# Optimization experiments

Measured on AMD Instinct MI355X. Metric: run time of the kernel, lower is better.

## Reference

```python
import jax, jax.numpy as jnp
import numpy as np

N = 200000; E = 800000; B = 4096; L = 512
DIN = 64; DE = 16; H = 128; PD = 1152


def setup_inputs() -> dict:
    key = jax.random.key(0)
    ks = jax.random.split(key, 40)
    def nrm(k, shape, fan_in):
        return jax.random.normal(k, shape, jnp.float32) * (1.0 / np.sqrt(fan_in))
    inp = {}
    inp['x'] = jax.random.normal(ks[0], (N, DIN), jnp.float32)
    inp['edge_index'] = jax.random.randint(ks[1], (2, E), 0, N, dtype=jnp.int32)
    inp['edge_attr'] = jax.random.normal(ks[2], (E, DE), jnp.float32)
    inp['batch'] = jnp.sort(jax.random.randint(ks[3], (N,), 0, B, dtype=jnp.int32))
    # 6 expert blocks: [0,1]=shared, [2,3]=sars, [4,5]=mers
    inp['eW1'] = nrm(ks[4], (6, DIN, H), DIN); inp['ea_s1'] = nrm(ks[5], (6, H), H)
    inp['ea_d1'] = nrm(ks[6], (6, H), H); inp['eWe1'] = nrm(ks[7], (6, DE, H), DE)
    inp['ea_e1'] = nrm(ks[8], (6, H), H); inp['eb1'] = jnp.zeros((6, H), jnp.float32)
    inp['bn1_g'] = jnp.ones((6, H), jnp.float32); inp['bn1_b'] = jnp.zeros((6, H), jnp.float32)
    inp['eW2'] = nrm(ks[9], (6, H, H), H); inp['ea_s2'] = nrm(ks[10], (6, H), H)
    inp['ea_d2'] = nrm(ks[11], (6, H), H); inp['eWe2'] = nrm(ks[12], (6, DE, H), DE)
    inp['ea_e2'] = nrm(ks[13], (6, H), H); inp['eb2'] = jnp.zeros((6, H), jnp.float32)
    inp['bn2_g'] = jnp.ones((6, H), jnp.float32); inp['bn2_b'] = jnp.zeros((6, H), jnp.float32)
    # gates (one GATConv with 4 output channels per task)
    inp['gW'] = nrm(ks[14], (2, DIN, 4), DIN); inp['ga_s'] = nrm(ks[15], (2, 4), 4)
    inp['ga_d'] = nrm(ks[16], (2, 4), 4); inp['gWe'] = nrm(ks[17], (2, DE, 4), DE)
    inp['ga_e'] = nrm(ks[18], (2, 4), 4); inp['gb'] = jnp.zeros((2, 4), jnp.float32)
    # cross-modal attention per task + frozen protein embeddings
    inp['Wq'] = nrm(ks[19], (2, H, H), H)
    inp['Wk'] = nrm(ks[20], (2, PD, H), PD)
    inp['Wv'] = nrm(ks[21], (2, PD, H), PD)
    inp['pe'] = jax.random.normal(ks[22], (2, L, PD), jnp.float32)
    # task heads
    inp['Wh1'] = nrm(ks[23], (2, 2 * H, H), 2 * H); inp['bh1'] = jnp.zeros((2, H), jnp.float32)
    inp['hbn_g'] = jnp.ones((2, H), jnp.float32); inp['hbn_b'] = jnp.zeros((2, H), jnp.float32)
    inp['Wh2'] = nrm(ks[24], (2, H, 1), H); inp['bh2'] = jnp.zeros((2, 1), jnp.float32)
    return inp


def _gat(x, src, dst, eattr, W, a_s, a_d, We, a_e, b):
    # PyG GATConv (heads=1, edge_dim set): shared linear for src/dst.
    h = x @ W                                   # [N, C]
    l = (h @ a_s)[src] + (h @ a_d)[dst] + (eattr @ We) @ a_e  # [E]
    l = jax.nn.leaky_relu(l, 0.2)
    m = jax.ops.segment_max(l, dst, num_segments=N)
    m = jnp.where(jnp.isfinite(m), m, 0.0)
    ex = jnp.exp(l - m[dst])
    den = jax.ops.segment_sum(ex, dst, num_segments=N)
    alpha = ex / (den[dst] + 1e-16)             # edge softmax over incoming edges
    return jax.ops.segment_sum(alpha[:, None] * h[src], dst, num_segments=N) + b


def _gat_multi(x, src, dst, eattr, W, a_s, a_d, We, a_e, b):
    # gate GATConv outputs C>1 channels with heads=1 -> same scalar-alpha math
    return _gat(x, src, dst, eattr, W, a_s, a_d, We, a_e, b)


def _bn(x, g, b):
    mu = jnp.mean(x, axis=0)
    var = jnp.var(x, axis=0)
    return (x - mu) * jax.lax.rsqrt(var + 1e-5) * g + b


def reference(x, edge_index, edge_attr, batch,
              eW1, ea_s1, ea_d1, eWe1, ea_e1, eb1, bn1_g, bn1_b,
              eW2, ea_s2, ea_d2, eWe2, ea_e2, eb2, bn2_g, bn2_b,
              gW, ga_s, ga_d, gWe, ga_e, gb,
              Wq, Wk, Wv, pe, Wh1, bh1, hbn_g, hbn_b, Wh2, bh2):
    src, dst = edge_index[0], edge_index[1]

    def expert(i):
        h = _gat(x, src, dst, edge_attr, eW1[i], ea_s1[i], ea_d1[i], eWe1[i], ea_e1[i], eb1[i])
        h = jax.nn.leaky_relu(_bn(h, bn1_g[i], bn1_b[i]), 0.01)
        h = _gat(h, src, dst, edge_attr, eW2[i], ea_s2[i], ea_d2[i], eWe2[i], ea_e2[i], eb2[i])
        return jax.nn.leaky_relu(_bn(h, bn2_g[i], bn2_b[i]), 0.01)

    reps = [expert(i) for i in range(6)]  # each [N, H]

    preds = []
    for t in range(2):
        # merged experts: shared then task-specific (cat order in torch code)
        merged = jnp.stack([reps[0], reps[1], reps[2 + 2 * t], reps[3 + 2 * t]], axis=1)  # [N,4,H]
        glog = _gat_multi(x, src, dst, edge_attr, gW[t], ga_s[t], ga_d[t], gWe[t], ga_e[t], gb[t])
        gate = jax.nn.softmax(glog, axis=1)                     # [N,4]
        node = jnp.einsum('neh,ne->nh', merged, gate)           # CGC combine
        pooled = jax.ops.segment_sum(node, batch, num_segments=B)  # global_add_pool [B,H]
        Q = pooled @ Wq[t]                                      # [B,H]
        K = pe[t] @ Wk[t]                                       # [L,H]
        V = pe[t] @ Wv[t]
        attn = jax.nn.softmax(Q @ K.T / jnp.sqrt(jnp.float32(H)), axis=-1)
        ctx = attn @ V
        fused = jnp.concatenate([pooled, ctx], axis=1)          # [B,2H]
        hh = jax.nn.leaky_relu(_bn(fused @ Wh1[t] + bh1[t], hbn_g[t], hbn_b[t]), 0.01)
        preds.append(hh @ Wh2[t] + bh2[t])
    return jnp.concatenate(preds, axis=1)  # [B,2]
```

## Files before the change

kernel.cpp:

```cpp
#include <hip/hip_runtime.h>
#include <hip/hip_bf16.h>
#include <cstdint>
#include <cstddef>
#include <type_traits>

constexpr int DIN = 64;
constexpr int DE  = 16;
constexpr int H   = 128;
constexpr int L   = 512;
constexpr int PD  = 1152;
constexpr int NAGG = 2048;

using bf16 = __hip_bfloat16;
typedef __attribute__((ext_vector_type(8))) short short8;
typedef __attribute__((ext_vector_type(4))) float float4v;

__device__ __forceinline__ float bflo(unsigned u) { return __uint_as_float(u << 16); }
__device__ __forceinline__ float bfhi(unsigned u) { return __uint_as_float(u & 0xffff0000u); }
__device__ __forceinline__ unsigned short f2b(float f) {
  bf16 h = __float2bfloat16(f);
  return *reinterpret_cast<unsigned short*>(&h);
}
__device__ __forceinline__ unsigned pack2(float a, float b) {
  return (unsigned)f2b(a) | ((unsigned)f2b(b) << 16);
}

__global__ void k_zero_i32(int* p, int n) {
  int i = blockIdx.x * 256 + threadIdx.x;
  if (i < n) p[i] = 0;
}
__global__ void k_zero_f32(float* p, int n) {
  int i = blockIdx.x * 256 + threadIdx.x;
  if (i < n) p[i] = 0.f;
}

__global__ void k_cvt_bf16(const float* __restrict__ in, bf16* __restrict__ out, int npairs) {
  int i = blockIdx.x * 256 + threadIdx.x;
  if (i >= npairs) return;
  float2 v = ((const float2*)in)[i];
  ((unsigned*)out)[i] = pack2(v.x, v.y);
}

__global__ void k_deg(const int* __restrict__ dst, int* __restrict__ deg, int e) {
  int i = blockIdx.x * 256 + threadIdx.x;
  if (i < e) atomicAdd(&deg[dst[i]], 1);
}

__global__ void k_scan1(const int* __restrict__ deg, int* __restrict__ out,
                        int* __restrict__ bsum, int n) {
  __shared__ int tmp[512];
  int tid = threadIdx.x;
  int i = blockIdx.x * 512 + tid;
  int v = (i < n) ? deg[i] : 0;
  tmp[tid] = v; __syncthreads();
  for (int s = 1; s < 512; s <<= 1) {
    int t = (tid >= s) ? tmp[tid - s] : 0;
    __syncthreads();
    tmp[tid] += t;
    __syncthreads();
  }
  if (i < n) out[i] = tmp[tid] - v;
  if (tid == 511) bsum[blockIdx.x] = tmp[511];
}

__global__ void k_scan2(int* bsum, int nb) {
  __shared__ int tmp[512];
  int tid = threadIdx.x;
  int v = (tid < nb) ? bsum[tid] : 0;
  tmp[tid] = v; __syncthreads();
  for (int s = 1; s < 512; s <<= 1) {
    int t = (tid >= s) ? tmp[tid - s] : 0;
    __syncthreads();
    tmp[tid] += t;
    __syncthreads();
  }
  if (tid < nb) bsum[tid] = tmp[tid] - v;
}

__global__ void k_scan3(int* __restrict__ off, const int* __restrict__ bsum,
                        int* __restrict__ cursor, int n, int total) {
  int i = blockIdx.x * 512 + threadIdx.x;
  if (i < n) { int v = off[i] + bsum[blockIdx.x]; off[i] = v; cursor[i] = v; }
  if (i == 0) off[n] = total;
}

__global__ void k_fill(const int* __restrict__ dst, int* __restrict__ cursor,
                       int* __restrict__ eid, int e) {
  int i = blockIdx.x * 256 + threadIdx.x;
  if (i < e) { int slot = atomicAdd(&cursor[dst[i]], 1); eid[slot] = i; }
}

__global__ void k_weall(const float* __restrict__ gWe, const float* __restrict__ ga_e,
                        const float* __restrict__ eWe1, const float* __restrict__ ea_e1,
                        const float* __restrict__ eWe2, const float* __restrict__ ea_e2,
                        float* __restrict__ weall) {
  int tid = threadIdx.x;
  if (tid >= 14 * 16) return;
  int c = tid >> 4, j = tid & 15;
  float acc = 0.f;
  if (c < 2) {
    for (int k = 0; k < 4; ++k) acc += gWe[(c * 16 + j) * 4 + k] * ga_e[c * 4 + k];
  } else if (c < 8) {
    int i = c - 2;
    for (int k = 0; k < 128; ++k) acc += eWe1[(i * 16 + j) * 128 + k] * ea_e1[i * 128 + k];
  } else {
    int i = c - 8;
    for (int k = 0; k < 128; ++k) acc += eWe2[(i * 16 + j) * 128 + k] * ea_e2[i * 128 + k];
  }
  weall[c * 16 + j] = acc;
}

__global__ void k_wpackall(const float* __restrict__ eW1, const float* __restrict__ eW2,
                           bf16* __restrict__ Wp1, bf16* __restrict__ Wp2) {
  int tid = blockIdx.x * 256 + threadIdx.x;
  const int L1TOT = 6 * 8192;
  if (tid < L1TOT) {
    int i = tid / 8192, r = tid % 8192;
    int kt = r / 4096, nt = (r / 512) & 7, l = (r / 8) & 63, j = r & 7;
    int k = kt * 32 + (l >> 4) * 8 + j, col = nt * 16 + (l & 15);
    Wp1[tid] = __float2bfloat16(eW1[(size_t)i * 64 * 128 + k * 128 + col]);
  } else {
    int t2 = tid - L1TOT;
    if (t2 >= 6 * 16384) return;
    int i = t2 / 16384, r = t2 % 16384;
    int kt = r / 4096, nt = (r / 512) & 7, l = (r / 8) & 63, j = r & 7;
    int k = kt * 32 + (l >> 4) * 8 + j, col = nt * 16 + (l & 15);
    Wp2[t2] = __float2bfloat16(eW2[(size_t)i * 128 * 128 + k * 128 + col]);
  }
}

__global__ void k_csrprep(const int* __restrict__ eid, const int* __restrict__ src,
                          const int* __restrict__ dst, const float* __restrict__ eattr,
                          const float* __restrict__ weall, int* __restrict__ src_csr,
                          int* __restrict__ dst_csr, float* __restrict__ edots, int e) {
  __shared__ float w[14 * 16];
  if (threadIdx.x < 14 * 16) w[threadIdx.x] = weall[threadIdx.x];
  __syncthreads();
  int i = blockIdx.x * 256 + threadIdx.x;
  if (i >= e) return;
  int ed = eid[i];
  src_csr[i] = src[ed];
  dst_csr[i] = dst[ed];
  float ea[16];
  const float4* ep = (const float4*)(eattr + (size_t)ed * 16);
#pragma unroll
  for (int q = 0; q < 4; ++q) {
    float4 v = ep[q];
    ea[q * 4] = v.x; ea[q * 4 + 1] = v.y; ea[q * 4 + 2] = v.z; ea[q * 4 + 3] = v.w;
  }
#pragma unroll
  for (int c = 0; c < 14; ++c) {
    float acc = 0.f;
#pragma unroll
    for (int j = 0; j < 16; ++j) acc += ea[j] * w[c * 16 + j];
    edots[(size_t)c * e + i] = acc;
  }
}

template <int K, bool BN>
__global__ __launch_bounds__(256) void k_mfma_gemm(
    const bf16* __restrict__ A, const bf16* __restrict__ Wp,
    const float* __restrict__ a_s, const float* __restrict__ a_d,
    bf16* __restrict__ out, float* __restrict__ s, float* __restrict__ d, int n,
    const float* __restrict__ bnsums, const float* __restrict__ bng,
    const float* __restrict__ bnb, float invn) {
  constexpr int KT = K / 32;
  __shared__ bf16 At[64][K + 8];
  __shared__ float sscale[128], sshift[128];
  if (BN) {
    if (threadIdx.x < K) {
      int c = threadIdx.x;
      float mu = bnsums[c] * invn;
      float var = bnsums[128 + c] * invn - mu * mu;
      float sc = rsqrtf(var + 1e-5f) * bng[c];
      sscale[c] = sc;
      sshift[c] = bnb[c] - mu * sc;
    }
    __syncthreads();
  }
  int row0 = blockIdx.x * 64;
  const int vecPerRow = K / 8;
  for (int idx = threadIdx.x; idx < 64 * vecPerRow; idx += 256) {
    int r = idx / vecPerRow, v = idx - r * vecPerRow;
    int gr = row0 + r;
    uint4 u = {0u, 0u, 0u, 0u};
    if (gr < n) u = ((const uint4*)(A + (size_t)gr * K))[v];
    if (BN) {
      float f[8] = {bflo(u.x), bfhi(u.x), bflo(u.y), bfhi(u.y),
                    bflo(u.z), bfhi(u.z), bflo(u.w), bfhi(u.w)};
      int c0 = v * 8;
#pragma unroll
      for (int j = 0; j < 8; ++j) {
        float y = f[j] * sscale[c0 + j] + sshift[c0 + j];
        f[j] = (y > 0.f) ? y : 0.01f * y;
      }
      u.x = pack2(f[0], f[1]); u.y = pack2(f[2], f[3]);
      u.z = pack2(f[4], f[5]); u.w = pack2(f[6], f[7]);
    }
    *((uint4*)&At[r][v * 8]) = u;
  }
  __syncthreads();
  int lane = threadIdx.x & 63, w = threadIdx.x >> 6;
  int c = lane & 15, q = lane >> 4;
  int wrow = w * 16;
  short8 afrag[KT];
#pragma unroll
  for (int kt = 0; kt < KT; ++kt)
    afrag[kt] = *(const short8*)&At[wrow + c][kt * 32 + q * 8];
  const short8* wp8 = (const short8*)Wp;
  float4v acc[8];
#pragma unroll
  for (int nt = 0; nt < 8; ++nt) acc[nt] = {0.f, 0.f, 0.f, 0.f};
#pragma unroll
  for (int kt = 0; kt < KT; ++kt) {
#pragma unroll
    for (int nt = 0; nt < 8; ++nt) {
      short8 bfrag = wp8[(kt * 8 + nt) * 64 + lane];
      acc[nt] = __builtin_amdgcn_mfma_f32_16x16x32_bf16(afrag[kt], bfrag, acc[nt], 0, 0, 0);
    }
  }
#pragma unroll
  for (int nt = 0; nt < 8; ++nt) {
#pragma unroll
    for (int reg = 0; reg < 4; ++reg) {
      int gr = row0 + wrow + q * 4 + reg;
      if (gr < n) out[(size_t)gr * 128 + nt * 16 + c] = __float2bfloat16(acc[nt][reg]);
    }
  }
#pragma unroll
  for (int reg = 0; reg < 4; ++reg) {
    float vs = 0.f, vd = 0.f;
#pragma unroll
    for (int nt = 0; nt < 8; ++nt) {
      float y = acc[nt][reg];
      int col = nt * 16 + c;
      vs += y * a_s[col];
      vd += y * a_d[col];
    }
#pragma unroll
    for (int o = 1; o < 16; o <<= 1) { vs += __shfl_xor(vs, o); vd += __shfl_xor(vd, o); }
    int gr = row0 + wrow + q * 4 + reg;
    if (c == 0 && gr < n) { s[gr] = vs; d[gr] = vd; }
  }
}

__global__ void k_edge_l(const int* __restrict__ src_csr, const int* __restrict__ dst_csr,
                         const float* __restrict__ edot, const float* __restrict__ s,
                         const float* __restrict__ d, float* __restrict__ lcsr, int e) {
  int i = blockIdx.x * 256 + threadIdx.x;
  if (i >= e) return;
  float l = s[src_csr[i]] + d[dst_csr[i]] + edot[i];
  lcsr[i] = (l > 0.f) ? l : 0.2f * l;
}

__global__ __launch_bounds__(256) void k_agg128s(
    const int* __restrict__ off, const int* __restrict__ src_csr,
    const float* __restrict__ lcsr, const bf16* __restrict__ feat,
    const float* __restrict__ bias, bf16* __restrict__ out,
    float* __restrict__ partials, int n) {
  __shared__ float sm[4][128], sq[4][128];
  int w = threadIdx.x >> 6, lane = threadIdx.x & 63;
  int g = lane >> 4, h = lane & 15;
  float b8[8];
#pragma unroll
  for (int j = 0; j < 8; ++j) b8[j] = bias[h * 8 + j];
  float sum8[8], sq8[8];
#pragma unroll
  for (int j = 0; j < 8; ++j) { sum8[j] = 0.f; sq8[j] = 0.f; }
  int stride = gridDim.x * 4;
  for (int node = blockIdx.x * 4 + w; node < n; node += stride) {
    int e0 = off[node], e1 = off[node + 1];
    float m = -INFINITY;
    for (int i = e0 + lane; i < e1; i += 64) m = fmaxf(m, lcsr[i]);
#pragma unroll
    for (int o = 32; o; o >>= 1) m = fmaxf(m, __shfl_xor(m, o));
    float den = 0.f;
    for (int i = e0 + lane; i < e1; i += 64) den += __expf(lcsr[i] - m);
#pragma unroll
    for (int o = 32; o; o >>= 1) den += __shfl_xor(den, o);
    float inv = 1.f / (den + 1e-16f);
    float acc[8];
#pragma unroll
    for (int j = 0; j < 8; ++j) acc[j] = 0.f;
    for (int i = e0 + g; i < e1; i += 4) {
      float alpha = __expf(lcsr[i] - m) * inv;
      uint4 u = ((const uint4*)(feat + (size_t)src_csr[i] * 128))[h];
      acc[0] += alpha * bflo(u.x); acc[1] += alpha * bfhi(u.x);
      acc[2] += alpha * bflo(u.y); acc[3] += alpha * bfhi(u.y);
      acc[4] += alpha * bflo(u.z); acc[5] += alpha * bfhi(u.z);
      acc[6] += alpha * bflo(u.w); acc[7] += alpha * bfhi(u.w);
    }
#pragma unroll
    for (int j = 0; j < 8; ++j) {
      acc[j] += __shfl_xor(acc[j], 16);
      acc[j] += __shfl_xor(acc[j], 32);
      acc[j] += b8[j];
    }
    if (g == 0) {
      uint4 o4;
      o4.x = pack2(acc[0], acc[1]); o4.y = pack2(acc[2], acc[3]);
      o4.z = pack2(acc[4], acc[5]); o4.w = pack2(acc[6], acc[7]);
      ((uint4*)(out + (size_t)node * 128))[h] = o4;
#pragma unroll
      for (int j = 0; j < 8; ++j) { sum8[j] += acc[j]; sq8[j] += acc[j] * acc[j]; }
    }
  }
  if (g == 0) {
#pragma unroll
    for (int j = 0; j < 8; ++j) { sm[w][h * 8 + j] = sum8[j]; sq[w][h * 8 + j] = sq8[j]; }
  }
  __syncthreads();
  if (threadIdx.x < 128) {
    int c = threadIdx.x;
    float a = sm[0][c] + sm[1][c] + sm[2][c] + sm[3][c];
    float b = sq[0][c] + sq[1][c] + sq[2][c] + sq[3][c];
    partials[(size_t)blockIdx.x * 256 + c] = a;
    partials[(size_t)blockIdx.x * 256 + 128 + c] = b;
  }
}

__global__ void k_gfeat(const float* __restrict__ x, const float* __restrict__ W,
                        const float* __restrict__ a_s, const float* __restrict__ a_d,
                        float* __restrict__ gfeat, float* __restrict__ s,
                        float* __restrict__ d, int n) {
  int i = blockIdx.x * 256 + threadIdx.x;
  if (i >= n) return;
  const float* xr = x + (size_t)i * DIN;
  float acc[4] = {0.f, 0.f, 0.f, 0.f};
  for (int k = 0; k < DIN; ++k) {
    float xv = xr[k];
#pragma unroll
    for (int j = 0; j < 4; ++j) acc[j] += xv * W[k * 4 + j];
  }
  float ss = 0.f, dd = 0.f;
#pragma unroll
  for (int j = 0; j < 4; ++j) {
    gfeat[(size_t)i * 4 + j] = acc[j];
    ss += acc[j] * a_s[j];
    dd += acc[j] * a_d[j];
  }
  s[i] = ss; d[i] = dd;
}

__global__ void k_agg4(const int* __restrict__ off, const int* __restrict__ src_csr,
                       const float* __restrict__ lcsr, const float* __restrict__ gfeat,
                       const float* __restrict__ bias, float* __restrict__ gates, int n) {
  int node = blockIdx.x * 256 + threadIdx.x;
  if (node >= n) return;
  int e0 = off[node], e1 = off[node + 1];
  float m = -INFINITY;
  for (int i = e0; i < e1; ++i) m = fmaxf(m, lcsr[i]);
  float den = 0.f;
  for (int i = e0; i < e1; ++i) den += __expf(lcsr[i] - m);
  float inv = 1.f / (den + 1e-16f);
  float4 acc = {0.f, 0.f, 0.f, 0.f};
  for (int i = e0; i < e1; ++i) {
    float a = __expf(lcsr[i] - m) * inv;
    float4 fr = *((const float4*)(gfeat + (size_t)src_csr[i] * 4));
    acc.x += a * fr.x; acc.y += a * fr.y; acc.z += a * fr.z; acc.w += a * fr.w;
  }
  float b0 = bias[0], b1 = bias[1], b2 = bias[2], b3 = bias[3];
  acc.x += b0; acc.y += b1; acc.z += b2; acc.w += b3;
  float mm = fmaxf(fmaxf(acc.x, acc.y), fmaxf(acc.z, acc.w));
  float e0s = __expf(acc.x - mm), e1s = __expf(acc.y - mm);
  float e2s = __expf(acc.z - mm), e3s = __expf(acc.w - mm);
  float is = 1.f / (e0s + e1s + e2s + e3s);
  float4 g4 = {e0s * is, e1s * is, e2s * is, e3s * is};
  *((float4*)(gates + (size_t)node * 4)) = g4;
}

__global__ void k_bnstats_fin(const float* __restrict__ partials, float* __restrict__ sums,
                              int nblk) {
  int t = threadIdx.x;
  int cl = t >> 5, sl = t & 31;
  int ch = blockIdx.x * 8 + cl;
  float a = 0.f, b = 0.f;
  for (int blk = sl; blk < nblk; blk += 32) {
    a += partials[(size_t)blk * 256 + ch];
    b += partials[(size_t)blk * 256 + 128 + ch];
  }
#pragma unroll
  for (int o = 16; o; o >>= 1) { a += __shfl_xor(a, o); b += __shfl_xor(b, o); }
  if (sl == 0) { sums[ch] = a; sums[128 + ch] = b; }
}

__global__ void k_bnstats_f32(const float* __restrict__ x, float* __restrict__ sums,
                              float* __restrict__ sumsq, int n) {
  __shared__ float s1[256], s2[256];
  int c = threadIdx.x & 127, half = threadIdx.x >> 7;
  float a = 0.f, b = 0.f;
  for (int r = blockIdx.x * 2 + half; r < n; r += gridDim.x * 2) {
    float v = x[(size_t)r * 128 + c];
    a += v; b += v * v;
  }
  s1[threadIdx.x] = a; s2[threadIdx.x] = b;
  __syncthreads();
  if (half == 0) {
    atomicAdd(&sums[c], s1[c] + s1[c + 128]);
    atomicAdd(&sumsq[c], s2[c] + s2[c + 128]);
  }
}

__global__ void k_poolexpert(const bf16* __restrict__ x, const float* __restrict__ sums,
                             const float* __restrict__ sumsq, const float* __restrict__ g,
                             const float* __restrict__ bb, const int* __restrict__ batch,
                             const float* __restrict__ gates0, int slot0,
                             const float* __restrict__ gates1, int slot1,
                             float* __restrict__ pooled0, float* __restrict__ pooled1,
                             int n, float invn) {
  int b = blockIdx.x, t = threadIdx.x;
  int lo = 0, hi = n;
  while (lo < hi) { int m = (lo + hi) >> 1; if (batch[m] < b) lo = m + 1; else hi = m; }
  int start = lo;
  lo = start; hi = n;
  while (lo < hi) { int m = (lo + hi) >> 1; if (batch[m] < b + 1) lo = m + 1; else hi = m; }
  int end = lo;
  int c0 = 2 * t, c1 = 2 * t + 1;
  float mu0 = sums[c0] * invn, mu1 = sums[c1] * invn;
  float sc0 = rsqrtf(sumsq[c0] * invn - mu0 * mu0 + 1e-5f) * g[c0];
  float sc1 = rsqrtf(sumsq[c1] * invn - mu1 * mu1 + 1e-5f) * g[c1];
  float sh0 = bb[c0], sh1 = bb[c1];
  float a00 = 0.f, a01 = 0.f, a10 = 0.f, a11 = 0.f;
  for (int r = start; r < end; ++r) {
    unsigned u = ((const unsigned*)(x + (size_t)r * 128))[t];
    float y0 = (bflo(u) - mu0) * sc0 + sh0;
    float y1 = (bfhi(u) - mu1) * sc1 + sh1;
    y0 = (y0 > 0.f) ? y0 : 0.01f * y0;
    y1 = (y1 > 0.f) ? y1 : 0.01f * y1;
    if (slot0 >= 0) {
      float gw = gates0[(size_t)r * 4 + slot0];
      a00 += gw * y0; a01 += gw * y1;
    }
    if (slot1 >= 0) {
      float gw = gates1[(size_t)r * 4 + slot1];
      a10 += gw * y0; a11 += gw * y1;
    }
  }
  if (slot0 >= 0) {
    pooled0[(size_t)b * 128 + c0] += a00;
    pooled0[(size_t)b * 128 + c1] += a01;
  }
  if (slot1 >= 0) {
    pooled1[(size_t)b * 128 + c0] += a10;
    pooled1[(size_t)b * 128 + c1] += a11;
  }
}

__global__ void k_kv(const float* __restrict__ pe, const float* __restrict__ Wk,
                     const float* __restrict__ Wv, float* __restrict__ Kt,
                     float* __restrict__ Vout) {
  __shared__ float per[PD];
  int l = blockIdx.x, c = threadIdx.x;
  for (int p = threadIdx.x; p < PD; p += 128) per[p] = pe[(size_t)l * PD + p];
  __syncthreads();
  float ak = 0.f, av = 0.f;
  for (int p = 0; p < PD; ++p) {
    float v = per[p];
    ak += v * Wk[p * 128 + c];
    av += v * Wv[p * 128 + c];
  }
  Kt[(size_t)c * L + l] = ak;
  Vout[(size_t)l * 128 + c] = av;
}

__global__ void k_rowgemm(const float* __restrict__ in, const float* __restrict__ W,
                          float* __restrict__ out, int Kdim) {
  __shared__ float rr[256];
  int row = blockIdx.x, c = threadIdx.x;
  for (int k = threadIdx.x; k < Kdim; k += 128) rr[k] = in[(size_t)row * Kdim + k];
  __syncthreads();
  float acc = 0.f;
  for (int k = 0; k < Kdim; ++k) acc += rr[k] * W[k * 128 + c];
  out[(size_t)row * 128 + c] = acc;
}

__global__ void k_attn(const float* __restrict__ Q, const float* __restrict__ Kt,
                       const float* __restrict__ Vm, float* __restrict__ ctx) {
  __shared__ float q[4][128];
  __shared__ float sc[4][L];
  __shared__ float4 red[128];
  __shared__ float4 Mg, Ig;
  int b0 = blockIdx.x * 4, t = threadIdx.x;
#pragma unroll
  for (int g = 0; g < 4; ++g) q[g][t] = Q[(size_t)(b0 + g) * 128 + t];
  __syncthreads();
  float acc[4][4];
#pragma unroll
  for (int g = 0; g < 4; ++g)
#pragma unroll
    for (int j = 0; j < 4; ++j) acc[g][j] = 0.f;
  for (int k = 0; k < 128; ++k) {
    const float* kr = Kt + (size_t)k * L + t;
    float k0 = kr[0], k1 = kr[128], k2 = kr[256], k3 = kr[384];
#pragma unroll
    for (int g = 0; g < 4; ++g) {
      float qv = q[g][k];
      acc[g][0] += qv * k0; acc[g][1] += qv * k1;
      acc[g][2] += qv * k2; acc[g][3] += qv * k3;
    }
  }
  const float scale = 0.08838834764831845f;
  float4 pm;
  {
    float m[4];
#pragma unroll
    for (int g = 0; g < 4; ++g) {
#pragma unroll
      for (int j = 0; j < 4; ++j) {
        acc[g][j] *= scale;
        sc[g][t + j * 128] = acc[g][j];
      }
      m[g] = fmaxf(fmaxf(acc[g][0], acc[g][1]), fmaxf(acc[g][2], acc[g][3]));
    }
    pm = {m[0], m[1], m[2], m[3]};
  }
  red[t] = pm; __syncthreads();
  for (int s = 64; s > 0; s >>= 1) {
    if (t < s) {
      float4 o = red[t + s];
      red[t].x = fmaxf(red[t].x, o.x); red[t].y = fmaxf(red[t].y, o.y);
      red[t].z = fmaxf(red[t].z, o.z); red[t].w = fmaxf(red[t].w, o.w);
    }
    __syncthreads();
  }
  if (t == 0) Mg = red[0];
  __syncthreads();
  float4 M = Mg;
  float4 ps = {0, 0, 0, 0};
#pragma unroll
  for (int g = 0; g < 4; ++g) {
    float mg = (g == 0) ? M.x : (g == 1) ? M.y : (g == 2) ? M.z : M.w;
    float sgsum = 0.f;
#pragma unroll
    for (int j = 0; j < 4; ++j) {
      float e = __expf(acc[g][j] - mg);
      sc[g][t + j * 128] = e;
      sgsum += e;
    }
    if (g == 0) ps.x = sgsum; else if (g == 1) ps.y = sgsum;
    else if (g == 2) ps.z = sgsum; else ps.w = sgsum;
  }
  __syncthreads();
  red[t] = ps; __syncthreads();
  for (int s = 64; s > 0; s >>= 1) {
    if (t < s) {
      float4 o = red[t + s];
      red[t].x += o.x; red[t].y += o.y; red[t].z += o.z; red[t].w += o.w;
    }
    __syncthreads();
  }
  if (t == 0) Ig = {1.f / red[0].x, 1.f / red[0].y, 1.f / red[0].z, 1.f / red[0].w};
  __syncthreads();
  float4 I = Ig;
  float o0 = 0.f, o1 = 0.f, o2 = 0.f, o3 = 0.f;
  for (int l = 0; l < L; ++l) {
    float v = Vm[(size_t)l * 128 + t];
    o0 += sc[0][l] * v; o1 += sc[1][l] * v; o2 += sc[2][l] * v; o3 += sc[3][l] * v;
  }
  ctx[(size_t)(b0 + 0) * 128 + t] = o0 * I.x;
  ctx[(size_t)(b0 + 1) * 128 + t] = o1 * I.y;
  ctx[(size_t)(b0 + 2) * 128 + t] = o2 * I.z;
  ctx[(size_t)(b0 + 3) * 128 + t] = o3 * I.w;
}

__global__ void k_head1(const float* __restrict__ pooled, const float* __restrict__ ctx,
                        const float* __restrict__ Wh1, const float* __restrict__ bh1,
                        float* __restrict__ hh) {
  __shared__ float f[256];
  int b = blockIdx.x, c = threadIdx.x;
  f[c] = pooled[(size_t)b * 128 + c];
  f[c + 128] = ctx[(size_t)b * 128 + c];
  __syncthreads();
  float acc = bh1[c];
  for (int k = 0; k < 256; ++k) acc += f[k] * Wh1[k * 128 + c];
  hh[(size_t)b * 128 + c] = acc;
}

__global__ void k_head2(const float* __restrict__ hh, const float* __restrict__ sums,
                        const float* __restrict__ sumsq, const float* __restrict__ g,
                        const float* __restrict__ bbn, const float* __restrict__ Wh2,
                        const float* __restrict__ bh2, float* __restrict__ out, int t,
                        float invn) {
  __shared__ float red[2];
  int b = blockIdx.x, c = threadIdx.x;
  float mu = sums[c] * invn;
  float var = sumsq[c] * invn - mu * mu;
  float y = (hh[(size_t)b * 128 + c] - mu) * rsqrtf(var + 1e-5f) * g[c] + bbn[c];
  y = (y > 0.f) ? y : 0.01f * y;
  float p = y * Wh2[c];
  for (int o = 32; o; o >>= 1) p += __shfl_down(p, o);
  if ((threadIdx.x & 63) == 0) red[threadIdx.x >> 6] = p;
  __syncthreads();
  if (threadIdx.x == 0) out[(size_t)b * 2 + t] = red[0] + red[1] + bh2[0];
}

extern "C" void kernel_launch(void* const* d_in, const int* in_sizes, int n_in,
                              void* d_out, int out_size, void* d_ws, size_t ws_size,
                              hipStream_t stream) {
  (void)n_in; (void)ws_size;
  const float* x     = (const float*)d_in[0];
  const int*   eidx  = (const int*)d_in[1];
  const float* eattr = (const float*)d_in[2];
  const int*   batch = (const int*)d_in[3];
  const float* eW1   = (const float*)d_in[4];
  const float* ea_s1 = (const float*)d_in[5];
  const float* ea_d1 = (const float*)d_in[6];
  const float* eWe1  = (const float*)d_in[7];
  const float* ea_e1 = (const float*)d_in[8];
  const float* eb1   = (const float*)d_in[9];
  const float* bn1_g = (const float*)d_in[10];
  const float* bn1_b = (const float*)d_in[11];
  const float* eW2   = (const float*)d_in[12];
  const float* ea_s2 = (const float*)d_in[13];
  const float* ea_d2 = (const float*)d_in[14];
  const float* eWe2  = (const float*)d_in[15];
  const float* ea_e2 = (const float*)d_in[16];
  const float* eb2   = (const float*)d_in[17];
  const float* bn2_g = (const float*)d_in[18];
  const float* bn2_b = (const float*)d_in[19];
  const float* gW    = (const float*)d_in[20];
  const float* ga_s  = (const float*)d_in[21];
  const float* ga_d  = (const float*)d_in[22];
  const float* gWe   = (const float*)d_in[23];
  const float* ga_e  = (const float*)d_in[24];
  const float* gb    = (const float*)d_in[25];
  const float* Wq    = (const float*)d_in[26];
  const float* Wk    = (const float*)d_in[27];
  const float* Wv    = (const float*)d_in[28];
  const float* pe    = (const float*)d_in[29];
  const float* Wh1   = (const float*)d_in[30];
  const float* bh1   = (const float*)d_in[31];
  const float* hbn_g = (const float*)d_in[32];
  const float* hbn_b = (const float*)d_in[33];
  const float* Wh2   = (const float*)d_in[34];
  const float* bh2   = (const float*)d_in[35];
  float* out = (float*)d_out;

  const int n = in_sizes[0] / DIN;
  const int e = in_sizes[1] / 2;
  const int nb_graphs = out_size / 2;
  const int* src = eidx;
  const int* dst = eidx + e;

  char* p = (char*)d_ws;
  auto carve = [&](size_t bytes) {
    void* r = (void*)p;
    p += (bytes + 255) & ~(size_t)255;
    return r;
  };
  int* deg       = (int*)carve((size_t)n * 4);
  int* off       = (int*)carve(((size_t)n + 1) * 4);
  int* cursor    = (int*)carve((size_t)n * 4);
  int* eid       = (int*)carve((size_t)e * 4);
  int* bsum      = (int*)carve(4096);
  int* src_csr   = (int*)carve((size_t)e * 4);
  int* dst_csr   = (int*)carve((size_t)e * 4);
  float* edots   = (float*)carve((size_t)14 * e * 4);
  float* weall   = (float*)carve(14 * 16 * 4);
  float* s_arr   = (float*)carve((size_t)n * 4);
  float* d_arr   = (float*)carve((size_t)n * 4);
  float* lcsr    = (float*)carve((size_t)e * 4);
  float* sums    = (float*)carve(256 * 4);
  float* partials = (float*)carve((size_t)NAGG * 256 * 4);
  float* gates0  = (float*)carve((size_t)n * 16);
  float* gates1  = (float*)carve((size_t)n * 16);
  float* gfeat   = (float*)carve((size_t)n * 16);
  float* pooled0 = (float*)carve((size_t)nb_graphs * H * 4);
  float* pooled1 = (float*)carve((size_t)nb_graphs * H * 4);
  float* Ktbuf   = (float*)carve((size_t)L * H * 4);
  float* Vbuf    = (float*)carve((size_t)L * H * 4);
  float* Qbuf    = (float*)carve((size_t)nb_graphs * H * 4);
  float* ctxb    = (float*)carve((size_t)nb_graphs * H * 4);
  float* hhb     = (float*)carve((size_t)nb_graphs * H * 4);
  bf16* featbuf  = (bf16*)carve((size_t)n * H * 2);
  bf16* buf1     = (bf16*)carve((size_t)n * H * 2);
  bf16* xbf      = (bf16*)carve((size_t)n * DIN * 2);
  bf16* Wp1      = (bf16*)carve((size_t)6 * 8192 * 2);
  bf16* Wp2      = (bf16*)carve((size_t)6 * 16384 * 2);

  float invn = 1.0f / n;

  k_cvt_bf16<<<(n * DIN / 2 + 255) / 256, 256, 0, stream>>>(x, xbf, n * DIN / 2);
  k_wpackall<<<(6 * 8192 + 6 * 16384 + 255) / 256, 256, 0, stream>>>(eW1, eW2, Wp1, Wp2);

  k_zero_i32<<<(n + 255) / 256, 256, 0, stream>>>(deg, n);
  k_deg<<<(e + 255) / 256, 256, 0, stream>>>(dst, deg, e);
  int nsb = (n + 511) / 512;
  k_scan1<<<nsb, 512, 0, stream>>>(deg, off, bsum, n);
  k_scan2<<<1, 512, 0, stream>>>(bsum, nsb);
  k_scan3<<<nsb, 512, 0, stream>>>(off, bsum, cursor, n, e);
  k_fill<<<(e + 255) / 256, 256, 0, stream>>>(dst, cursor, eid, e);

  k_weall<<<1, 256, 0, stream>>>(gWe, ga_e, eWe1, ea_e1, eWe2, ea_e2, weall);
  k_csrprep<<<(e + 255) / 256, 256, 0, stream>>>(eid, src, dst, eattr, weall, src_csr,
                                                 dst_csr, edots, e);

  for (int t = 0; t < 2; ++t) {
    float* gates = t ? gates1 : gates0;
    k_gfeat<<<(n + 255) / 256, 256, 0, stream>>>(x, gW + t * DIN * 4, ga_s + t * 4,
                                                 ga_d + t * 4, gfeat, s_arr, d_arr, n);
    k_edge_l<<<(e + 255) / 256, 256, 0, stream>>>(src_csr, dst_csr, edots + (size_t)t * e,
                                                  s_arr, d_arr, lcsr, e);
    k_agg4<<<(n + 255) / 256, 256, 0, stream>>>(off, src_csr, lcsr, gfeat, gb + t * 4,
                                                gates, n);
  }

  k_zero_f32<<<(nb_graphs * H + 255) / 256, 256, 0, stream>>>(pooled0, nb_graphs * H);
  k_zero_f32<<<(nb_graphs * H + 255) / 256, 256, 0, stream>>>(pooled1, nb_graphs * H);

  int gblk = (n + 63) / 64;
  for (int i = 0; i < 6; ++i) {
    k_mfma_gemm<DIN, false><<<gblk, 256, 0, stream>>>(
        xbf, Wp1 + (size_t)i * 8192, ea_s1 + i * H, ea_d1 + i * H, featbuf, s_arr, d_arr,
        n, nullptr, nullptr, nullptr, 0.f);
    k_edge_l<<<(e + 255) / 256, 256, 0, stream>>>(src_csr, dst_csr,
                                                  edots + (size_t)(2 + i) * e, s_arr,
                                                  d_arr, lcsr, e);
    k_agg128s<<<NAGG, 256, 0, stream>>>(off, src_csr, lcsr, featbuf, eb1 + i * H, buf1,
                                        partials, n);
    k_bnstats_fin<<<16, 256, 0, stream>>>(partials, sums, NAGG);
    k_mfma_gemm<H, true><<<gblk, 256, 0, stream>>>(
        buf1, Wp2 + (size_t)i * 16384, ea_s2 + i * H, ea_d2 + i * H, featbuf, s_arr,
        d_arr, n, sums, bn1_g + i * H, bn1_b + i * H, invn);
    k_edge_l<<<(e + 255) / 256, 256, 0, stream>>>(src_csr, dst_csr,
                                                  edots + (size_t)(8 + i) * e, s_arr,
                                                  d_arr, lcsr, e);
    k_agg128s<<<NAGG, 256, 0, stream>>>(off, src_csr, lcsr, featbuf, eb2 + i * H, buf1,
                                        partials, n);
    k_bnstats_fin<<<16, 256, 0, stream>>>(partials, sums, NAGG);
    int s0 = (i < 4) ? i : -1;
    int s1 = (i < 2) ? i : (i >= 4 ? i - 2 : -1);
    k_poolexpert<<<nb_graphs, 64, 0, stream>>>(buf1, sums, sums + 128, bn2_g + i * H,
                                               bn2_b + i * H, batch, gates0, s0, gates1,
                                               s1, pooled0, pooled1, n, invn);
  }

  for (int t = 0; t < 2; ++t) {
    const float* pooled = t ? pooled1 : pooled0;
    k_kv<<<L, 128, 0, stream>>>(pe + (size_t)t * L * PD, Wk + t * PD * H, Wv + t * PD * H,
                                Ktbuf, Vbuf);
    k_rowgemm<<<nb_graphs, 128, 0, stream>>>(pooled, Wq + t * H * H, Qbuf, H);
    k_attn<<<nb_graphs / 4, 128, 0, stream>>>(Qbuf, Ktbuf, Vbuf, ctxb);
    k_head1<<<nb_graphs, 128, 0, stream>>>(pooled, ctxb, Wh1 + t * 2 * H * H, bh1 + t * H,
                                           hhb);
    k_zero_f32<<<1, 256, 0, stream>>>(sums, 256);
    k_bnstats_f32<<<64, 256, 0, stream>>>(hhb, sums, sums + 128, nb_graphs);
    k_head2<<<nb_graphs, 128, 0, stream>>>(hhb, sums, sums + 128, hbn_g + t * H,
                                           hbn_b + t * H, Wh2 + t * H, bh2 + t, out, t,
                                           1.0f / nb_graphs);
  }
}
```

Measured before the change: 3.199 ms.

## Precompute softmax alphas per node and aggregate with half-wave per node

Edge softmax normalisation moves into a separate per-node kernel that writes normalised alphas in place. The 128-wide aggregation then maps one 32-lane group to each node, each lane handling 4 channels, with no max/sum reductions or cross-lane combining. The aggregation grid doubles so each block covers 8 nodes per iteration. This adds an extra kernel launch and an extra pass over the edge logits, with serial per-thread loops over each node's edges, in exchange for less wasted lane work when degrees are low (around 4 on average).

```diff
diff --git a/kernel.cpp b/kernel.cpp
--- a/kernel.cpp
+++ b/kernel.cpp
@@ -9,7 +9,7 @@
 constexpr int H   = 128;
 constexpr int L   = 512;
 constexpr int PD  = 1152;
-constexpr int NAGG = 2048;
+constexpr int NAGG = 4096;
 
 using bf16 = __hip_bfloat16;
 typedef __attribute__((ext_vector_type(8))) short short8;
@@ -253,67 +253,63 @@
   lcsr[i] = (l > 0.f) ? l : 0.2f * l;
 }
 
-__global__ __launch_bounds__(256) void k_agg128s(
+__global__ void k_nodealpha(const int* __restrict__ off, float* __restrict__ lcsr, int n) {
+  int node = blockIdx.x * 256 + threadIdx.x;
+  if (node >= n) return;
+  int e0 = off[node], e1 = off[node + 1];
+  if (e0 == e1) return;
+  float m = -INFINITY;
+  for (int i = e0; i < e1; ++i) m = fmaxf(m, lcsr[i]);
+  float den = 0.f;
+  for (int i = e0; i < e1; ++i) {
+    float ex = __expf(lcsr[i] - m);
+    lcsr[i] = ex;
+    den += ex;
+  }
+  float inv = 1.f / (den + 1e-16f);
+  for (int i = e0; i < e1; ++i) lcsr[i] *= inv;
+}
+
+__global__ __launch_bounds__(256) void k_agg128v(
     const int* __restrict__ off, const int* __restrict__ src_csr,
-    const float* __restrict__ lcsr, const bf16* __restrict__ feat,
+    const float* __restrict__ alpha, const bf16* __restrict__ feat,
     const float* __restrict__ bias, bf16* __restrict__ out,
     float* __restrict__ partials, int n) {
-  __shared__ float sm[4][128], sq[4][128];
-  int w = threadIdx.x >> 6, lane = threadIdx.x & 63;
-  int g = lane >> 4, h = lane & 15;
-  float b8[8];
-#pragma unroll
-  for (int j = 0; j < 8; ++j) b8[j] = bias[h * 8 + j];
-  float sum8[8], sq8[8];
-#pragma unroll
-  for (int j = 0; j < 8; ++j) { sum8[j] = 0.f; sq8[j] = 0.f; }
-  int stride = gridDim.x * 4;
-  for (int node = blockIdx.x * 4 + w; node < n; node += stride) {
+  __shared__ float sm[8][128], sq2[8][128];
+  int grp = threadIdx.x >> 5, lane = threadIdx.x & 31;
+  float4 b4 = ((const float4*)bias)[lane];
+  float s0 = 0.f, s1 = 0.f, s2 = 0.f, s3 = 0.f;
+  float q0 = 0.f, q1 = 0.f, q2 = 0.f, q3 = 0.f;
+  int stride = gridDim.x * 8;
+  for (int node = blockIdx.x * 8 + grp; node < n; node += stride) {
     int e0 = off[node], e1 = off[node + 1];
-    float m = -INFINITY;
-    for (int i = e0 + lane; i < e1; i += 64) m = fmaxf(m, lcsr[i]);
-#pragma unroll
-    for (int o = 32; o; o >>= 1) m = fmaxf(m, __shfl_xor(m, o));
-    float den = 0.f;
-    for (int i = e0 + lane; i < e1; i += 64) den += __expf(lcsr[i] - m);
-#pragma unroll
-    for (int o = 32; o; o >>= 1) den += __shfl_xor(den, o);
-    float inv = 1.f / (den + 1e-16f);
-    float acc[8];
-#pragma unroll
-    for (int j = 0; j < 8; ++j) acc[j] = 0.f;
-    for (int i = e0 + g; i < e1; i += 4) {
-      float alpha = __expf(lcsr[i] - m) * inv;
-      uint4 u = ((const uint4*)(feat + (size_t)src_csr[i] * 128))[h];
-      acc[0] += alpha * bflo(u.x); acc[1] += alpha * bfhi(u.x);
-      acc[2] += alpha * bflo(u.y); acc[3] += alpha * bfhi(u.y);
-      acc[4] += alpha * bflo(u.z); acc[5] += alpha * bfhi(u.z);
-      acc[6] += alpha * bflo(u.w); acc[7] += alpha * bfhi(u.w);
-    }
-#pragma unroll
-    for (int j = 0; j < 8; ++j) {
-      acc[j] += __shfl_xor(acc[j], 16);
-      acc[j] += __shfl_xor(acc[j], 32);
-      acc[j] += b8[j];
-    }
-    if (g == 0) {
-      uint4 o4;
-      o4.x = pack2(acc[0], acc[1]); o4.y = pack2(acc[2], acc[3]);
-      o4.z = pack2(acc[4], acc[5]); o4.w = pack2(acc[6], acc[7]);
-      ((uint4*)(out + (size_t)node * 128))[h] = o4;
-#pragma unroll
-      for (int j = 0; j < 8; ++j) { sum8[j] += acc[j]; sq8[j] += acc[j] * acc[j]; }
-    }
-  }
-  if (g == 0) {
-#pragma unroll
-    for (int j = 0; j < 8; ++j) { sm[w][h * 8 + j] = sum8[j]; sq[w][h * 8 + j] = sq8[j]; }
-  }
+    float a0 = 0.f, a1 = 0.f, a2 = 0.f, a3 = 0.f;
+    for (int i = e0; i < e1; ++i) {
+      float al = alpha[i];
+      uint2 u = ((const uint2*)(feat + (size_t)src_csr[i] * 128))[lane];
+      a0 += al * bflo(u.x);
+      a1 += al * bfhi(u.x);
+      a2 += al * bflo(u.y);
+      a3 += al * bfhi(u.y);
+    }
+    a0 += b4.x; a1 += b4.y; a2 += b4.z; a3 += b4.w;
+    uint2 o2;
+    o2.x = pack2(a0, a1);
+    o2.y = pack2(a2, a3);
+    ((uint2*)(out + (size_t)node * 128))[lane] = o2;
+    s0 += a0; s1 += a1; s2 += a2; s3 += a3;
+    q0 += a0 * a0; q1 += a1 * a1; q2 += a2 * a2; q3 += a3 * a3;
+  }
+  sm[grp][lane * 4] = s0; sm[grp][lane * 4 + 1] = s1;
+  sm[grp][lane * 4 + 2] = s2; sm[grp][lane * 4 + 3] = s3;
+  sq2[grp][lane * 4] = q0; sq2[grp][lane * 4 + 1] = q1;
+  sq2[grp][lane * 4 + 2] = q2; sq2[grp][lane * 4 + 3] = q3;
   __syncthreads();
   if (threadIdx.x < 128) {
     int c = threadIdx.x;
-    float a = sm[0][c] + sm[1][c] + sm[2][c] + sm[3][c];
-    float b = sq[0][c] + sq[1][c] + sq[2][c] + sq[3][c];
+    float a = 0.f, b = 0.f;
+#pragma unroll
+    for (int g = 0; g < 8; ++g) { a += sm[g][c]; b += sq2[g][c]; }
     partials[(size_t)blockIdx.x * 256 + c] = a;
     partials[(size_t)blockIdx.x * 256 + 128 + c] = b;
   }
@@ -716,7 +712,8 @@
     k_edge_l<<<(e + 255) / 256, 256, 0, stream>>>(src_csr, dst_csr,
                                                   edots + (size_t)(2 + i) * e, s_arr,
                                                   d_arr, lcsr, e);
-    k_agg128s<<<NAGG, 256, 0, stream>>>(off, src_csr, lcsr, featbuf, eb1 + i * H, buf1,
+    k_nodealpha<<<(n + 255) / 256, 256, 0, stream>>>(off, lcsr, n);
+    k_agg128v<<<NAGG, 256, 0, stream>>>(off, src_csr, lcsr, featbuf, eb1 + i * H, buf1,
                                         partials, n);
     k_bnstats_fin<<<16, 256, 0, stream>>>(partials, sums, NAGG);
     k_mfma_gemm<H, true><<<gblk, 256, 0, stream>>>(
@@ -725,7 +722,8 @@
     k_edge_l<<<(e + 255) / 256, 256, 0, stream>>>(src_csr, dst_csr,
                                                   edots + (size_t)(8 + i) * e, s_arr,
                                                   d_arr, lcsr, e);
-    k_agg128s<<<NAGG, 256, 0, stream>>>(off, src_csr, lcsr, featbuf, eb2 + i * H, buf1,
+    k_nodealpha<<<(n + 255) / 256, 256, 0, stream>>>(off, lcsr, n);
+    k_agg128v<<<NAGG, 256, 0, stream>>>(off, src_csr, lcsr, featbuf, eb2 + i * H, buf1,
                                         partials, n);
     k_bnstats_fin<<<16, 256, 0, stream>>>(partials, sums, NAGG);
     int s0 = (i < 4) ? i : -1;
```

After: 2.895 ms. 1.11x faster.
